# Optimization experiments

Hardware: AMD Instinct MI355X
Metric: run time of the kernel (lower is better)

## Reference

```python
import jax, jax.numpy as jnp
import numpy as np

THETA = 10000.0
D_K = 128
MAX_SEQ_LEN = 8192
BATCH, HEADS, SEQ = 4, 16, 4096


def setup_inputs() -> dict:
    key = jax.random.key(0)
    kx, = jax.random.split(key, 1)
    x = jax.random.normal(kx, (BATCH, HEADS, SEQ, D_K), dtype=jnp.float32)
    token_positions = jnp.arange(SEQ, dtype=jnp.int32)  # broadcast over batch dims
    # Precompute the same angles the torch module bakes into its block-diag
    # rotation matrices: angle[i, k] = i / theta ** (2k / d_k)
    k = jnp.arange(D_K // 2, dtype=jnp.float32)
    inv_freq = THETA ** (-2.0 * k / D_K)                      # [d_k/2]
    pos = jnp.arange(MAX_SEQ_LEN, dtype=jnp.float32)          # [max_seq_len]
    angles = pos[:, None] * inv_freq[None, :]                 # [max_seq_len, d_k/2]
    cos_table = jnp.cos(angles)
    sin_table = jnp.sin(angles)
    return {"x": x, "token_positions": token_positions,
            "cos_table": cos_table, "sin_table": sin_table}


def reference(x, token_positions, cos_table, sin_table):
    # Gather per-position cos/sin: (..., seq, d_k/2). Mathematically identical
    # to gathering the [d_k, d_k] block-diag rotation matrix and doing a matvec,
    # since each 2x2 block rotates an interleaved pair (x[2k], x[2k+1]).
    c = cos_table[token_positions]
    s = sin_table[token_positions]
    xp = x.reshape(x.shape[:-1] + (D_K // 2, 2))   # (..., seq, d_k/2, 2)
    x1, x2 = xp[..., 0], xp[..., 1]
    o1 = c * x1 - s * x2
    o2 = s * x1 + c * x2
    return jnp.stack((o1, o2), axis=-1).reshape(x.shape)
```

## Files before the change

### kernel.cpp

```cpp
#include <hip/hip_runtime.h>


constexpr int SEQ      = 4096;
constexpr int D_K      = 128;
constexpr int F4_PER_ROW = D_K / 4;

__global__ __launch_bounds__(256) void rope_kernel(
    const float4* __restrict__ x,
    const int*    __restrict__ tok_pos,
    const float2* __restrict__ cos_t,
    const float2* __restrict__ sin_t,
    float4*       __restrict__ out)
{
    const int i = blockIdx.x * blockDim.x + threadIdx.x;

    const int within = i & (F4_PER_ROW - 1);
    const int row    = i >> 5;
    const int s      = row & (SEQ - 1);
    const int p      = tok_pos[s];

    const float2 c  = cos_t[p * (D_K / 4) + within];
    const float2 sn = sin_t[p * (D_K / 4) + within];

    const float4 v = x[i];
    float4 o;
    o.x = c.x * v.x - sn.x * v.y;
    o.y = sn.x * v.x + c.x * v.y;
    o.z = c.y * v.z - sn.y * v.w;
    o.w = sn.y * v.z + c.y * v.w;
    out[i] = o;
}

extern "C" void kernel_launch(void* const* d_in, const int* in_sizes, int n_in,
                              void* d_out, int out_size, void* d_ws, size_t ws_size,
                              hipStream_t stream) {
    const float4* x       = (const float4*)d_in[0];
    const int*    tok_pos = (const int*)d_in[1];
    const float2* cos_t   = (const float2*)d_in[2];
    const float2* sin_t   = (const float2*)d_in[3];
    float4*       out     = (float4*)d_out;

    const int n4 = out_size / 4;
    const int block = 256;
    const int grid  = n4 / block;

    rope_kernel<<<grid, block, 0, stream>>>(x, tok_pos, cos_t, sin_t, out);
}
```

Measured before the change: 227.4 us.

## Process 8 floats per thread with unrolled grid stride and nontemporal loads/stores

Each thread now handles 8 elements (two float4 vectors) sharing one float4 cos/sin load, and loops over 4 chunks per thread with a grid stride. Loads of x and stores of out use nontemporal builtins so the streamed data does not pollute cache. The aim is fewer threads, fewer table loads per element and better memory-level parallelism for this bandwidth-bound kernel. Each thread's two float4 accesses are adjacent rather than fully coalesced across lanes, which may change access efficiency.

```diff
diff --git a/kernel.cpp b/kernel.cpp
--- a/kernel.cpp
+++ b/kernel.cpp
@@ -1,48 +1,66 @@
 #include <hip/hip_runtime.h>
 
 
-constexpr int SEQ      = 4096;
-constexpr int D_K      = 128;
-constexpr int F4_PER_ROW = D_K / 4;
+typedef float f4 __attribute__((ext_vector_type(4)));
 
-__global__ __launch_bounds__(256) void rope_kernel(
-    const float4* __restrict__ x,
-    const int*    __restrict__ tok_pos,
-    const float2* __restrict__ cos_t,
-    const float2* __restrict__ sin_t,
-    float4*       __restrict__ out)
+constexpr int SEQ        = 4096;
+constexpr int D_K        = 128;
+constexpr int CH_PER_ROW = D_K / 8;
+constexpr int BLOCK      = 256;
+constexpr int UNROLL     = 4;
+
+__global__ __launch_bounds__(BLOCK) void rope_kernel(
+    const f4* __restrict__ x,
+    const int* __restrict__ tok_pos,
+    const f4* __restrict__ cos_t,
+    const f4* __restrict__ sin_t,
+    f4*       __restrict__ out,
+    const int n_chunks)
 {
-    const int i = blockIdx.x * blockDim.x + threadIdx.x;
+    const int tid    = blockIdx.x * BLOCK + threadIdx.x;
+    const int stride = gridDim.x * BLOCK;
 
-    const int within = i & (F4_PER_ROW - 1);
-    const int row    = i >> 5;
-    const int s      = row & (SEQ - 1);
-    const int p      = tok_pos[s];
+#pragma unroll
+    for (int u = 0; u < UNROLL; ++u) {
+        const int e = tid + u * stride;
+        if (e < n_chunks) {
+            const int w = e & (CH_PER_ROW - 1);
+            const int s = (e >> 4) & (SEQ - 1);
+            const int p = tok_pos[s];
 
-    const float2 c  = cos_t[p * (D_K / 4) + within];
-    const float2 sn = sin_t[p * (D_K / 4) + within];
+            const f4 c  = cos_t[p * CH_PER_ROW + w];
+            const f4 sn = sin_t[p * CH_PER_ROW + w];
 
-    const float4 v = x[i];
-    float4 o;
-    o.x = c.x * v.x - sn.x * v.y;
-    o.y = sn.x * v.x + c.x * v.y;
-    o.z = c.y * v.z - sn.y * v.w;
-    o.w = sn.y * v.z + c.y * v.w;
-    out[i] = o;
+            const f4 a = __builtin_nontemporal_load(&x[2 * e]);
+            const f4 b = __builtin_nontemporal_load(&x[2 * e + 1]);
+
+            f4 oa, ob;
+            oa.x = c.x * a.x - sn.x * a.y;
+            oa.y = sn.x * a.x + c.x * a.y;
+            oa.z = c.y * a.z - sn.y * a.w;
+            oa.w = sn.y * a.z + c.y * a.w;
+            ob.x = c.z * b.x - sn.z * b.y;
+            ob.y = sn.z * b.x + c.z * b.y;
+            ob.z = c.w * b.z - sn.w * b.w;
+            ob.w = sn.w * b.z + c.w * b.w;
+
+            __builtin_nontemporal_store(oa, &out[2 * e]);
+            __builtin_nontemporal_store(ob, &out[2 * e + 1]);
+        }
+    }
 }
 
 extern "C" void kernel_launch(void* const* d_in, const int* in_sizes, int n_in,
                               void* d_out, int out_size, void* d_ws, size_t ws_size,
                               hipStream_t stream) {
-    const float4* x       = (const float4*)d_in[0];
-    const int*    tok_pos = (const int*)d_in[1];
-    const float2* cos_t   = (const float2*)d_in[2];
-    const float2* sin_t   = (const float2*)d_in[3];
-    float4*       out     = (float4*)d_out;
+    const f4*  x       = (const f4*)d_in[0];
+    const int* tok_pos = (const int*)d_in[1];
+    const f4*  cos_t   = (const f4*)d_in[2];
+    const f4*  sin_t   = (const f4*)d_in[3];
+    f4*        out     = (f4*)d_out;
 
-    const int n4 = out_size / 4;
-    const int block = 256;
-    const int grid  = n4 / block;
+    const int n_chunks = out_size / 8;
+    const int grid = (n_chunks + BLOCK * UNROLL - 1) / (BLOCK * UNROLL);
 
-    rope_kernel<<<grid, block, 0, stream>>>(x, tok_pos, cos_t, sin_t, out);
+    rope_kernel<<<grid, BLOCK, 0, stream>>>(x, tok_pos, cos_t, sin_t, out, n_chunks);
 }
```

After: 241.0 us. +6.0%, slower.

## Precompute interleaved cos/sin table in workspace and stream x with nontemporal ops

Applied to the files above, without the earlier changes.

A prep kernel gathers cos/sin by token position into one interleaved float4 table in workspace. The main kernel then does one coalesced table load plus nontemporal loads and stores of x and out, with no index gather. This removes the tok_pos indirection and the two float2 loads per thread. In exchange it adds a second launch and a 2 MB table write and read each call, and falls back to the original kernel when workspace is too small.

```diff
diff --git a/kernel.cpp b/kernel.cpp
--- a/kernel.cpp
+++ b/kernel.cpp
@@ -1,29 +1,64 @@
 #include <hip/hip_runtime.h>
 
 
-constexpr int SEQ      = 4096;
-constexpr int D_K      = 128;
+typedef float f4 __attribute__((ext_vector_type(4)));
+typedef float f2 __attribute__((ext_vector_type(2)));
+
+constexpr int SEQ        = 4096;
+constexpr int D_K        = 128;
 constexpr int F4_PER_ROW = D_K / 4;
+constexpr int FUSED_F4   = SEQ * F4_PER_ROW;
+constexpr int BLOCK      = 256;
 
-__global__ __launch_bounds__(256) void rope_kernel(
-    const float4* __restrict__ x,
-    const int*    __restrict__ tok_pos,
-    const float2* __restrict__ cos_t,
-    const float2* __restrict__ sin_t,
-    float4*       __restrict__ out)
+__global__ __launch_bounds__(BLOCK) void rope_prep(
+    const int* __restrict__ tok_pos,
+    const f2*  __restrict__ cos_t,
+    const f2*  __restrict__ sin_t,
+    f4*        __restrict__ fused)
 {
-    const int i = blockIdx.x * blockDim.x + threadIdx.x;
+    const int i = blockIdx.x * BLOCK + threadIdx.x;
+    const int j = i & (F4_PER_ROW - 1);
+    const int s = i >> 5;
+    const int p = tok_pos[s];
+    const f2 c  = cos_t[p * F4_PER_ROW + j];
+    const f2 sn = sin_t[p * F4_PER_ROW + j];
+    f4 t;
+    t.x = c.x;  t.y = sn.x;  t.z = c.y;  t.w = sn.y;
+    fused[i] = t;
+}
 
+__global__ __launch_bounds__(BLOCK) void rope_main(
+    const f4* __restrict__ x,
+    const f4* __restrict__ fused,
+    f4*       __restrict__ out)
+{
+    const int i = blockIdx.x * BLOCK + threadIdx.x;
+    const f4 t = fused[i & (FUSED_F4 - 1)];
+    const f4 v = __builtin_nontemporal_load(&x[i]);
+    f4 o;
+    o.x = t.x * v.x - t.y * v.y;
+    o.y = t.y * v.x + t.x * v.y;
+    o.z = t.z * v.z - t.w * v.w;
+    o.w = t.w * v.z + t.z * v.w;
+    __builtin_nontemporal_store(o, &out[i]);
+}
+
+__global__ __launch_bounds__(BLOCK) void rope_fallback(
+    const f4* __restrict__ x,
+    const int* __restrict__ tok_pos,
+    const f2* __restrict__ cos_t,
+    const f2* __restrict__ sin_t,
+    f4*       __restrict__ out)
+{
+    const int i = blockIdx.x * BLOCK + threadIdx.x;
     const int within = i & (F4_PER_ROW - 1);
     const int row    = i >> 5;
     const int s      = row & (SEQ - 1);
     const int p      = tok_pos[s];
-
-    const float2 c  = cos_t[p * (D_K / 4) + within];
-    const float2 sn = sin_t[p * (D_K / 4) + within];
-
-    const float4 v = x[i];
-    float4 o;
+    const f2 c  = cos_t[p * F4_PER_ROW + within];
+    const f2 sn = sin_t[p * F4_PER_ROW + within];
+    const f4 v = x[i];
+    f4 o;
     o.x = c.x * v.x - sn.x * v.y;
     o.y = sn.x * v.x + c.x * v.y;
     o.z = c.y * v.z - sn.y * v.w;
@@ -34,15 +69,20 @@
 extern "C" void kernel_launch(void* const* d_in, const int* in_sizes, int n_in,
                               void* d_out, int out_size, void* d_ws, size_t ws_size,
                               hipStream_t stream) {
-    const float4* x       = (const float4*)d_in[0];
-    const int*    tok_pos = (const int*)d_in[1];
-    const float2* cos_t   = (const float2*)d_in[2];
-    const float2* sin_t   = (const float2*)d_in[3];
-    float4*       out     = (float4*)d_out;
+    const f4*  x       = (const f4*)d_in[0];
+    const int* tok_pos = (const int*)d_in[1];
+    const f2*  cos_t   = (const f2*)d_in[2];
+    const f2*  sin_t   = (const f2*)d_in[3];
+    f4*        out     = (f4*)d_out;
 
     const int n4 = out_size / 4;
-    const int block = 256;
-    const int grid  = n4 / block;
+    const int grid = n4 / BLOCK;
 
-    rope_kernel<<<grid, block, 0, stream>>>(x, tok_pos, cos_t, sin_t, out);
+    if (ws_size >= (size_t)FUSED_F4 * 16) {
+        f4* fused = (f4*)d_ws;
+        rope_prep<<<FUSED_F4 / BLOCK, BLOCK, 0, stream>>>(tok_pos, cos_t, sin_t, fused);
+        rope_main<<<grid, BLOCK, 0, stream>>>(x, fused, out);
+    } else {
+        rope_fallback<<<grid, BLOCK, 0, stream>>>(x, tok_pos, cos_t, sin_t, out);
+    }
 }
```

Result: no change. 228.5 us (+0.5%).
